# Optimization experiments

Measured on AMD Instinct MI355X. Metric: run time of the kernel, lower is better.

The kernel has to match this reference:

```python
import jax, jax.numpy as jnp
import numpy as np

B, N, A, H, HID = 2048, 8, 16, 32, 64   # batch, n_agents, dim_action, dim_utility_hidden, dim_hidden
DQ = (H + A) * N                         # dim_q_input


def setup_inputs() -> dict:
    key = jax.random.key(0)
    ks = jax.random.split(key, 6)
    def w(k, shape, fan_in):
        return jax.random.normal(k, shape, jnp.float32) / np.sqrt(fan_in).astype(np.float32)
    return {
        "hidden_states_n": jax.random.normal(ks[0], (B, N, H), jnp.float32),
        # one-hot actions, as QTRAN substitutes torch.eye(dim_action) rows
        "actions_n": jax.nn.one_hot(jax.random.randint(ks[1], (B, N), 0, A), A, dtype=jnp.float32),
        "q_w1": w(ks[2], (DQ, HID), DQ), "q_b1": jnp.zeros((HID,), jnp.float32),
        "q_w2": w(ks[3], (HID, HID), HID), "q_b2": jnp.zeros((HID,), jnp.float32),
        "q_w3": w(ks[4], (HID, 1), HID), "q_b3": jnp.zeros((1,), jnp.float32),
    }


def reference(hidden_states_n, actions_n, q_w1, q_b1, q_w2, q_b2, q_w3, q_b3):
    """Vectorized QTRAN_alt.counterfactual_values_hat.

    Original: for each agent g and action a, replace agent g's action with one-hot(a)
    and run the joint Q_jt MLP. Here all n_agents*dim_action substitutions are
    built by broadcasting and run as one batched MLP.
    Output: [B, n_agents, dim_action].
    """
    Bn, Nn, Hh = hidden_states_n.shape
    Aa = actions_n.shape[-1]
    eye_a = jnp.eye(Aa, dtype=actions_n.dtype)          # [a, dA]
    agent_eq = jnp.eye(Nn, dtype=bool)                  # [g, j]: j == g
    # cf_actions[b, g, a, j, :] = eye_a[a] if j == g else actions_n[b, j, :]
    cf_actions = jnp.where(
        agent_eq[None, :, None, :, None],               # [1,G,1,J,1]
        eye_a[None, None, :, None, :],                  # [1,1,A,1,dA]
        actions_n[:, None, None, :, :],                 # [B,1,1,J,dA]
    )                                                   # [B,G,A,J,dA]
    hid = jnp.broadcast_to(hidden_states_n[:, None, None, :, :], (Bn, Nn, Aa, Nn, Hh))
    # per-agent (hidden, action) concat then flatten agents, matching
    # torch.cat([h, a], -1).view([-1, dim_q_input])
    inp = jnp.concatenate([hid, cf_actions], axis=-1).reshape(Bn, Nn, Aa, Nn * (Hh + Aa))
    h1 = jax.nn.relu(inp @ q_w1 + q_b1)
    h2 = jax.nn.relu(h1 @ q_w2 + q_b2)
    q = h2 @ q_w3 + q_b3                                # [B, G, A, 1]
    return q[..., 0]
```

## Files before the change

### kernel.cpp

```cpp
#include <hip/hip_runtime.h>
#include <hip/hip_bf16.h>

typedef __attribute__((ext_vector_type(4))) float f32x4;
typedef __attribute__((ext_vector_type(8))) short bf16x8;
typedef __attribute__((ext_vector_type(4))) short s16x4;

#define H1S 72

struct Smem {
    float inp[384];
    float base[64];
    float sub[8][64];
    int   sel[8];
    union {
        float part[4][64];
        __align__(16) short h1[128 * H1S];
    } u;
};

template<bool ISF32>
__device__ __forceinline__ float ldin(const void* p, int i) {
    if constexpr (ISF32) return ((const float*)p)[i];
    else return __bfloat162float(((const __hip_bfloat16*)p)[i]);
}

template<bool ISF32>
__device__ __forceinline__ f32x4 ldq(const void* p, int i) {
    if constexpr (ISF32) return *(const f32x4*)((const float*)p + i);
    else {
        const __hip_bfloat16* q = (const __hip_bfloat16*)p + i;
        return (f32x4){__bfloat162float(q[0]), __bfloat162float(q[1]),
                       __bfloat162float(q[2]), __bfloat162float(q[3])};
    }
}

__device__ __forceinline__ short bf16bits(float v) {
    __hip_bfloat16 h = __float2bfloat16(v);
    return *(const short*)&h;
}
__device__ __forceinline__ float bf16val(short s) {
    return __bfloat162float(*(const __hip_bfloat16*)&s);
}

__device__ __forceinline__ bool word_looks_bf16(unsigned int w) {
    const unsigned int lo = w & 0xFFFFu;
    const unsigned int ex = (lo >> 7) & 0xFFu;
    return (ex >= 100u && ex <= 140u) || (lo & 0x7FFFu) == 0u;
}

__device__ __forceinline__ bool vote_isf32_scalar(const void* hidden) {
    const unsigned int* hw = (const unsigned int*)hidden;
    int cnt = 0;
    #pragma unroll
    for (int i = 0; i < 32; ++i) cnt += word_looks_bf16(hw[i]) ? 1 : 0;
    return cnt < 16;
}

template<bool ISF32>
__device__ void w2prep_body(const void* w2, short* wsfrag, int idx0) {
    #pragma unroll
    for (int i = 0; i < 2; ++i) {
        const int idx = idx0 + i * 2048;
        const int j = idx & 7;
        const int lane = (idx >> 3) & 63;
        const int nt = (idx >> 9) & 3;
        const int ks = idx >> 11;
        const int src = (ks * 32 + (lane >> 4) * 8 + j) * 64 + nt * 16 + (lane & 15);
        const float v = ldin<ISF32>(w2, src);
        const short hb = bf16bits(v);
        wsfrag[idx] = hb;
        wsfrag[4096 + idx] = bf16bits(v - bf16val(hb));
    }
}

__global__ __launch_bounds__(256) void w2prep_kernel(
    const void* __restrict__ hidden, const void* __restrict__ w2,
    short* __restrict__ wsfrag) {
    const int idx0 = blockIdx.x * 256 + threadIdx.x;
    if (vote_isf32_scalar(hidden)) w2prep_body<true>(w2, wsfrag, idx0);
    else                           w2prep_body<false>(w2, wsfrag, idx0);
}

template<bool ISF32>
__device__ void qtran_body(Smem& sm,
    const void* __restrict__ hidden, const void* __restrict__ actions,
    const void* __restrict__ w1, const void* __restrict__ b1,
    const void* __restrict__ w2, const void* __restrict__ b2,
    const void* __restrict__ w3, const void* __restrict__ b3,
    void* __restrict__ out, const short* __restrict__ wsfrag, int b, int t)
{
    const int lane = t & 63;
    const int wv = t >> 6;
    const int q = lane >> 4;
    const int n = lane & 15;
    const int fq = lane & 15;
    const int rofs = lane >> 4;

    if (t < 64) {
        const int j = t >> 3, k4 = (t & 7) * 4;
        *(f32x4*)&sm.inp[j * 48 + k4] = ldq<ISF32>(hidden, (b * 8 + j) * 32 + k4);
    } else if (t < 96) {
        const int i = t - 64;
        const int j = i >> 2, c4 = (i & 3) * 4;
        *(f32x4*)&sm.inp[j * 48 + 32 + c4] = ldq<ISF32>(actions, (b * 8 + j) * 16 + c4);
    }
    __syncthreads();

    if (t < 128) {
        const int g = t >> 4, a = t & 15;
        if (sm.inp[g * 48 + 32 + a] > 0.5f) sm.sel[g] = a;
    }

    {
        f32x4 a4 = (f32x4){0.f, 0.f, 0.f, 0.f};
        #pragma unroll 8
        for (int p = 0; p < 16; ++p) {
            const int hr = wv * 64 + p * 4 + rofs;
            const int r = (hr >> 5) * 48 + (hr & 31);
            const float xv = sm.inp[r];
            const f32x4 wq = ldq<ISF32>(w1, r * 64 + fq * 4);
            #pragma unroll
            for (int c = 0; c < 4; ++c) a4[c] = fmaf(xv, wq[c], a4[c]);
        }
        #pragma unroll
        for (int c = 0; c < 4; ++c) {
            a4[c] += __shfl_xor(a4[c], 16);
            a4[c] += __shfl_xor(a4[c], 32);
        }
        if (rofs == 0) *(f32x4*)&sm.u.part[wv][fq * 4] = a4;
    }
    __syncthreads();

    if (t < 128) {
        const int g = t >> 4, f4 = (t & 15) * 4;
        *(f32x4*)&sm.sub[g][f4] =
            ldq<ISF32>(w1, (g * 48 + 32 + sm.sel[g]) * 64 + f4);
    }
    else if (t >= 128 && t < 192) {
        const int f = t - 128;
        sm.base[f] = ldin<ISF32>(b1, f) + sm.u.part[0][f] + sm.u.part[1][f]
                   + sm.u.part[2][f] + sm.u.part[3][f];
    }
    __syncthreads();

    {
        const int itm = t >> 4;
        const int hfq = t & 15;
        f32x4 S = *(const f32x4*)&sm.sub[0][hfq * 4];
        #pragma unroll
        for (int g = 1; g < 8; ++g) {
            const f32x4 sg = *(const f32x4*)&sm.sub[g][hfq * 4];
            #pragma unroll
            for (int c = 0; c < 4; ++c) S[c] += sg[c];
        }
        f32x4 bs = *(const f32x4*)&sm.base[hfq * 4];
        #pragma unroll
        for (int c = 0; c < 4; ++c) bs[c] += S[c];
        #pragma unroll
        for (int p = 0; p < 8; ++p) {
            const int item = p * 16 + itm;
            const int g = item >> 4, a = item & 15;
            const f32x4 wq = ldq<ISF32>(w1, (g * 48 + 32 + a) * 64 + hfq * 4);
            const f32x4 sb = *(const f32x4*)&sm.sub[g][hfq * 4];
            s16x4 hi;
            #pragma unroll
            for (int c = 0; c < 4; ++c)
                hi[c] = bf16bits(fmaxf(bs[c] - sb[c] + wq[c], 0.f));
            *(s16x4*)&sm.u.h1[item * H1S + hfq * 4] = hi;
        }
    }
    __syncthreads();

    f32x4 acc[2][4];
    #pragma unroll
    for (int mt = 0; mt < 2; ++mt)
      #pragma unroll
      for (int nt = 0; nt < 4; ++nt)
        acc[mt][nt] = (f32x4){0.f, 0.f, 0.f, 0.f};

    #pragma unroll
    for (int ks = 0; ks < 2; ++ks) {
        bf16x8 ahi[2];
        #pragma unroll
        for (int mt = 0; mt < 2; ++mt) {
            const int item = wv * 32 + mt * 16 + n;
            ahi[mt] = *(const bf16x8*)&sm.u.h1[item * H1S + ks * 32 + q * 8];
        }
        #pragma unroll
        for (int nt = 0; nt < 4; ++nt) {
            bf16x8 bhi, blo;
            if (wsfrag) {
                const int fb = ((ks * 4 + nt) * 64 + lane) * 8;
                bhi = *(const bf16x8*)&wsfrag[fb];
                blo = *(const bf16x8*)&wsfrag[4096 + fb];
            } else {
                #pragma unroll
                for (int j = 0; j < 8; ++j) {
                    const float v = ldin<ISF32>(w2, (ks * 32 + q * 8 + j) * 64 + nt * 16 + n);
                    const short hb = bf16bits(v);
                    bhi[j] = hb;
                    blo[j] = bf16bits(v - bf16val(hb));
                }
            }
            #pragma unroll
            for (int mt = 0; mt < 2; ++mt) {
                acc[mt][nt] = __builtin_amdgcn_mfma_f32_16x16x32_bf16(
                    ahi[mt], bhi, acc[mt][nt], 0, 0, 0);
                acc[mt][nt] = __builtin_amdgcn_mfma_f32_16x16x32_bf16(
                    ahi[mt], blo, acc[mt][nt], 0, 0, 0);
            }
        }
    }

    float b2f[4], w3f[4];
    #pragma unroll
    for (int nt = 0; nt < 4; ++nt) {
        b2f[nt] = ldin<ISF32>(b2, nt * 16 + n);
        w3f[nt] = ldin<ISF32>(w3, nt * 16 + n);
    }
    const float b3f = ldin<ISF32>(b3, 0);

    #pragma unroll
    for (int mt = 0; mt < 2; ++mt) {
      #pragma unroll
      for (int r = 0; r < 4; ++r) {
        float p = 0.f;
        #pragma unroll
        for (int nt = 0; nt < 4; ++nt) {
            const float h2 = fmaxf(acc[mt][nt][r] + b2f[nt], 0.f);
            p = fmaf(h2, w3f[nt], p);
        }
        p += __shfl_xor(p, 1);
        p += __shfl_xor(p, 2);
        p += __shfl_xor(p, 4);
        p += __shfl_xor(p, 8);
        if (n == mt * 4 + r) {
            const int item = wv * 32 + mt * 16 + q * 4 + r;
            if constexpr (ISF32) ((float*)out)[b * 128 + item] = p + b3f;
            else ((__hip_bfloat16*)out)[b * 128 + item] = __float2bfloat16(p + b3f);
        }
      }
    }
}

__global__ __launch_bounds__(256, 6) void qtran_cf_kernel(
    const void* __restrict__ hidden, const void* __restrict__ actions,
    const void* __restrict__ w1, const void* __restrict__ b1,
    const void* __restrict__ w2, const void* __restrict__ b2,
    const void* __restrict__ w3, const void* __restrict__ b3,
    void* __restrict__ out, const short* __restrict__ wsfrag)
{
    __shared__ Smem sm;
    const unsigned int* hw = (const unsigned int*)hidden;
    const bool pass = word_looks_bf16(hw[threadIdx.x & 31]);
    const unsigned long long m = __ballot(pass);
    const bool isf32 = (__popcll(m) < 32);

    const int b = blockIdx.x;
    const int t = threadIdx.x;
    if (isf32)
        qtran_body<true>(sm, hidden, actions, w1, b1, w2, b2, w3, b3, out, wsfrag, b, t);
    else
        qtran_body<false>(sm, hidden, actions, w1, b1, w2, b2, w3, b3, out, wsfrag, b, t);
}

extern "C" void kernel_launch(void* const* d_in, const int* in_sizes, int n_in,
                              void* d_out, int out_size, void* d_ws, size_t ws_size,
                              hipStream_t stream) {
    short* wsfrag = (ws_size >= 16384) ? (short*)d_ws : nullptr;
    if (wsfrag)
        w2prep_kernel<<<8, 256, 0, stream>>>(d_in[0], d_in[4], wsfrag);
    qtran_cf_kernel<<<2048, 256, 0, stream>>>(
        d_in[0], d_in[1], d_in[2], d_in[3], d_in[4], d_in[5], d_in[6], d_in[7],
        d_out, wsfrag);
}
```

Measured before the change: 84.85 us.

## Build layer-1 activations directly in MFMA registers, drop LDS h1 staging

Layer-1 activations for each wave's items are now computed straight into the bf16 MFMA A-operand registers, with each lane holding the matching W1 action rows. This removes the h1 shared-memory round trip and one __syncthreads. The per-agent substitution sum is precomputed by an idle thread group, and the W1/b2/w3 loads are hoisted to the kernel start to overlap latency. In exchange, register pressure rises, so launch bounds drop from 6 to 4 blocks per SM, which may reduce occupancy.

```diff
diff --git a/kernel.cpp b/kernel.cpp
--- a/kernel.cpp
+++ b/kernel.cpp
@@ -3,19 +3,14 @@
 
 typedef __attribute__((ext_vector_type(4))) float f32x4;
 typedef __attribute__((ext_vector_type(8))) short bf16x8;
-typedef __attribute__((ext_vector_type(4))) short s16x4;
-
-#define H1S 72
 
 struct Smem {
     float inp[384];
+    float part[4][64];
     float base[64];
+    float subsum[64];
     float sub[8][64];
     int   sel[8];
-    union {
-        float part[4][64];
-        __align__(16) short h1[128 * H1S];
-    } u;
 };
 
 template<bool ISF32>
@@ -96,6 +91,24 @@
     const int fq = lane & 15;
     const int rofs = lane >> 4;
 
+    f32x4 wr[2][2][2];
+    #pragma unroll
+    for (int mt = 0; mt < 2; ++mt) {
+        const int row = ((wv * 2 + mt) * 48 + 32 + n) * 64;
+        #pragma unroll
+        for (int ks = 0; ks < 2; ++ks) {
+            wr[mt][ks][0] = ldq<ISF32>(w1, row + ks * 32 + q * 8);
+            wr[mt][ks][1] = ldq<ISF32>(w1, row + ks * 32 + q * 8 + 4);
+        }
+    }
+    float b2f[4], w3f[4];
+    #pragma unroll
+    for (int nt = 0; nt < 4; ++nt) {
+        b2f[nt] = ldin<ISF32>(b2, nt * 16 + n);
+        w3f[nt] = ldin<ISF32>(w3, nt * 16 + n);
+    }
+    const float b3f = ldin<ISF32>(b3, 0);
+
     if (t < 64) {
         const int j = t >> 3, k4 = (t & 7) * 4;
         *(f32x4*)&sm.inp[j * 48 + k4] = ldq<ISF32>(hidden, (b * 8 + j) * 32 + k4);
@@ -110,7 +123,6 @@
         const int g = t >> 4, a = t & 15;
         if (sm.inp[g * 48 + 32 + a] > 0.5f) sm.sel[g] = a;
     }
-
     {
         f32x4 a4 = (f32x4){0.f, 0.f, 0.f, 0.f};
         #pragma unroll 8
@@ -127,7 +139,7 @@
             a4[c] += __shfl_xor(a4[c], 16);
             a4[c] += __shfl_xor(a4[c], 32);
         }
-        if (rofs == 0) *(f32x4*)&sm.u.part[wv][fq * 4] = a4;
+        if (rofs == 0) *(f32x4*)&sm.part[wv][fq * 4] = a4;
     }
     __syncthreads();
 
@@ -135,41 +147,49 @@
         const int g = t >> 4, f4 = (t & 15) * 4;
         *(f32x4*)&sm.sub[g][f4] =
             ldq<ISF32>(w1, (g * 48 + 32 + sm.sel[g]) * 64 + f4);
-    }
-    else if (t >= 128 && t < 192) {
+    } else if (t < 192) {
         const int f = t - 128;
-        sm.base[f] = ldin<ISF32>(b1, f) + sm.u.part[0][f] + sm.u.part[1][f]
-                   + sm.u.part[2][f] + sm.u.part[3][f];
+        sm.base[f] = ldin<ISF32>(b1, f) + sm.part[0][f] + sm.part[1][f]
+                   + sm.part[2][f] + sm.part[3][f];
+    } else {
+        const int f = t - 192;
+        float s = 0.f;
+        #pragma unroll
+        for (int g = 0; g < 8; ++g)
+            s += ldin<ISF32>(w1, (g * 48 + 32 + sm.sel[g]) * 64 + f);
+        sm.subsum[f] = s;
     }
     __syncthreads();
 
-    {
-        const int itm = t >> 4;
-        const int hfq = t & 15;
-        f32x4 S = *(const f32x4*)&sm.sub[0][hfq * 4];
-        #pragma unroll
-        for (int g = 1; g < 8; ++g) {
-            const f32x4 sg = *(const f32x4*)&sm.sub[g][hfq * 4];
+    f32x4 bsA[2][2];
+    #pragma unroll
+    for (int ks = 0; ks < 2; ++ks)
+      #pragma unroll
+      for (int h = 0; h < 2; ++h) {
+        const int f0 = ks * 32 + q * 8 + h * 4;
+        const f32x4 bb = *(const f32x4*)&sm.base[f0];
+        const f32x4 ss = *(const f32x4*)&sm.subsum[f0];
+        bsA[ks][h] = (f32x4){bb[0] + ss[0], bb[1] + ss[1], bb[2] + ss[2], bb[3] + ss[3]};
+      }
+    bf16x8 ahi[2][2];
+    #pragma unroll
+    for (int mt = 0; mt < 2; ++mt) {
+        const int g = wv * 2 + mt;
+        #pragma unroll
+        for (int ks = 0; ks < 2; ++ks) {
             #pragma unroll
-            for (int c = 0; c < 4; ++c) S[c] += sg[c];
-        }
-        f32x4 bs = *(const f32x4*)&sm.base[hfq * 4];
-        #pragma unroll
-        for (int c = 0; c < 4; ++c) bs[c] += S[c];
-        #pragma unroll
-        for (int p = 0; p < 8; ++p) {
-            const int item = p * 16 + itm;
-            const int g = item >> 4, a = item & 15;
-            const f32x4 wq = ldq<ISF32>(w1, (g * 48 + 32 + a) * 64 + hfq * 4);
-            const f32x4 sb = *(const f32x4*)&sm.sub[g][hfq * 4];
-            s16x4 hi;
-            #pragma unroll
-            for (int c = 0; c < 4; ++c)
-                hi[c] = bf16bits(fmaxf(bs[c] - sb[c] + wq[c], 0.f));
-            *(s16x4*)&sm.u.h1[item * H1S + hfq * 4] = hi;
-        }
-    }
-    __syncthreads();
+            for (int h = 0; h < 2; ++h) {
+                const int f0 = ks * 32 + q * 8 + h * 4;
+                const f32x4 sg = *(const f32x4*)&sm.sub[g][f0];
+                const f32x4 w4 = wr[mt][ks][h];
+                #pragma unroll
+                for (int c = 0; c < 4; ++c) {
+                    const float v = fmaxf(bsA[ks][h][c] - sg[c] + w4[c], 0.f);
+                    ahi[ks][mt][h * 4 + c] = bf16bits(v);
+                }
+            }
+        }
+    }
 
     f32x4 acc[2][4];
     #pragma unroll
@@ -180,12 +200,6 @@
 
     #pragma unroll
     for (int ks = 0; ks < 2; ++ks) {
-        bf16x8 ahi[2];
-        #pragma unroll
-        for (int mt = 0; mt < 2; ++mt) {
-            const int item = wv * 32 + mt * 16 + n;
-            ahi[mt] = *(const bf16x8*)&sm.u.h1[item * H1S + ks * 32 + q * 8];
-        }
         #pragma unroll
         for (int nt = 0; nt < 4; ++nt) {
             bf16x8 bhi, blo;
@@ -205,20 +219,12 @@
             #pragma unroll
             for (int mt = 0; mt < 2; ++mt) {
                 acc[mt][nt] = __builtin_amdgcn_mfma_f32_16x16x32_bf16(
-                    ahi[mt], bhi, acc[mt][nt], 0, 0, 0);
+                    ahi[ks][mt], bhi, acc[mt][nt], 0, 0, 0);
                 acc[mt][nt] = __builtin_amdgcn_mfma_f32_16x16x32_bf16(
-                    ahi[mt], blo, acc[mt][nt], 0, 0, 0);
+                    ahi[ks][mt], blo, acc[mt][nt], 0, 0, 0);
             }
         }
     }
-
-    float b2f[4], w3f[4];
-    #pragma unroll
-    for (int nt = 0; nt < 4; ++nt) {
-        b2f[nt] = ldin<ISF32>(b2, nt * 16 + n);
-        w3f[nt] = ldin<ISF32>(w3, nt * 16 + n);
-    }
-    const float b3f = ldin<ISF32>(b3, 0);
 
     #pragma unroll
     for (int mt = 0; mt < 2; ++mt) {
@@ -243,7 +249,7 @@
     }
 }
 
-__global__ __launch_bounds__(256, 6) void qtran_cf_kernel(
+__global__ __launch_bounds__(256, 4) void qtran_cf_kernel(
     const void* __restrict__ hidden, const void* __restrict__ actions,
     const void* __restrict__ w1, const void* __restrict__ b1,
     const void* __restrict__ w2, const void* __restrict__ b2,
```

Result: slower. 90.26 us (+6.4%).
